# Performance work log

Measured on AMD Instinct MI355X. Metric: run time of the kernel, lower is better.

## Reference

```python
import jax, jax.numpy as jnp
import numpy as np
from jax import lax

DIM = 192
HEADS = 8
HID = int(DIM * 4.0)

def setup_inputs() -> dict:
    key = jax.random.key(0)
    ks = jax.random.split(key, 10)
    b, c, h, w = 4, DIM, 256, DIM  # w must equal dim for the Mlp over last axis
    x = jax.random.normal(ks[0], (b, c, h, w), dtype=jnp.float32)
    return {
        "x": x,
        "ln1_w": jnp.ones((DIM,), jnp.float32),
        "ln1_b": jnp.zeros((DIM,), jnp.float32),
        "temperature": jnp.ones((HEADS, 1, 1), jnp.float32),
        "qkv_w": jax.random.normal(ks[1], (3 * DIM, DIM), jnp.float32) * 0.02,
        "dw_w": jax.random.normal(ks[2], (3 * DIM, 1, 3, 3), jnp.float32) * 0.1,
        "proj_w": jax.random.normal(ks[3], (DIM, DIM), jnp.float32) * 0.02,
        "ln2_w": jnp.ones((DIM,), jnp.float32),
        "ln2_b": jnp.zeros((DIM,), jnp.float32),
        "fc1_w": jax.random.normal(ks[4], (HID, DIM), jnp.float32) * 0.02,
        "fc1_b": jnp.zeros((HID,), jnp.float32),
        "fc2_w": jax.random.normal(ks[5], (DIM, HID), jnp.float32) * 0.02,
        "fc2_b": jnp.zeros((DIM,), jnp.float32),
    }

def _layernorm_chan(x, w, b):
    # WithBias LayerNorm over the channel axis, per spatial location (to_3d -> LN -> to_4d)
    mu = jnp.mean(x, axis=1, keepdims=True)
    var = jnp.mean((x - mu) ** 2, axis=1, keepdims=True)
    y = (x - mu) / jnp.sqrt(var + 1e-5)
    return y * w[None, :, None, None] + b[None, :, None, None]

def _l2norm(x, axis=-1, eps=1e-12):
    n = jnp.sqrt(jnp.sum(x * x, axis=axis, keepdims=True))
    return x / jnp.maximum(n, eps)

def _attention(x, temperature, qkv_w, dw_w, proj_w):
    b, c, h, w = x.shape
    # 1x1 conv (pointwise GEMM) then 3x3 depthwise conv
    qkv = jnp.einsum('oc,bchw->bohw', qkv_w, x)
    qkv = lax.conv_general_dilated(qkv, dw_w, window_strides=(1, 1), padding='SAME',
                                   feature_group_count=3 * c,
                                   dimension_numbers=('NCHW', 'OIHW', 'NCHW'))
    q, k, v = jnp.split(qkv, 3, axis=1)
    ch = c // HEADS
    q = q.reshape(b, HEADS, ch, h * w)
    k = k.reshape(b, HEADS, ch, h * w)
    v = v.reshape(b, HEADS, ch, h * w)
    q = _l2norm(q)
    k = _l2norm(k)
    attn = jnp.einsum('bhcn,bhdn->bhcd', q, k) * temperature  # [b,H,ch,ch] channel attention
    attn = jax.nn.softmax(attn, axis=-1)
    out = jnp.einsum('bhcd,bhdn->bhcn', attn, v).reshape(b, c, h, w)
    return jnp.einsum('oc,bchw->bohw', proj_w, out)

def _mlp(x, fc1_w, fc1_b, fc2_w, fc2_b):
    # nn.Linear applied on the LAST axis (w == dim), matching the original quirk
    h1 = jnp.einsum('bchw,ow->bcho', x, fc1_w) + fc1_b
    h1 = jax.nn.gelu(h1, approximate=False)
    return jnp.einsum('bcho,do->bchd', h1, fc2_w) + fc2_b

def reference(x, ln1_w, ln1_b, temperature, qkv_w, dw_w, proj_w, ln2_w, ln2_b, fc1_w, fc1_b, fc2_w, fc2_b):
    x = x + _attention(_layernorm_chan(x, ln1_w, ln1_b), temperature, qkv_w, dw_w, proj_w)
    x = x + _mlp(_layernorm_chan(x, ln2_w, ln2_b), fc1_w, fc1_b, fc2_w, fc2_b)
    return x
```

## Files before the change

kernel.cpp:

```cpp
#include <hip/hip_runtime.h>
#include <math.h>

#define SSP   49152
#define HDIM  256
#define WDIM  192
#define CDIM  192
#define NHEAD 8
#define CH    24
#define OC3   576
#define HIDF  768
#define NB    4
#define SCCH  24

typedef short bf16x8 __attribute__((ext_vector_type(8)));
typedef short bf16x4 __attribute__((ext_vector_type(4)));
typedef float f32x4  __attribute__((ext_vector_type(4)));

__device__ inline short f2bf(float f) {
  unsigned u = __float_as_uint(f);
  u += 0x7fffu + ((u >> 16) & 1u);
  return (short)(u >> 16);
}
__device__ inline float bf2f(short h) {
  return __uint_as_float(((unsigned)(unsigned short)h) << 16);
}

__device__ inline void gl_lds16(const short* g, short* l) {
  __builtin_amdgcn_global_load_lds(
      (const __attribute__((address_space(1))) unsigned int*)g,
      (__attribute__((address_space(3))) unsigned int*)l, 16, 0, 0);
}

__global__ __launch_bounds__(256) void cvt_bf16(const float* __restrict__ in,
                                                short* __restrict__ out, int n) {
  int i = blockIdx.x * 256 + threadIdx.x;
  if (i < n) out[i] = f2bf(in[i]);
}

template <bool TRANS>
__global__ __launch_bounds__(256) void ln_bf16(const float* __restrict__ x,
                                               const float* __restrict__ w,
                                               const float* __restrict__ bia,
                                               short* __restrict__ outp) {
  __shared__ float xs[192][68];
  __shared__ float ps[4][64], pq[4][64], mus[64], rst[64];
  const int tid = threadIdx.x;
  const int s0 = blockIdx.x * 64;
  const float* xb = x + (size_t)blockIdx.y * CDIM * SSP;
  short* outb = outp + (size_t)blockIdx.y * CDIM * SSP;
#pragma unroll
  for (int it = 0; it < 12; ++it) {
    int u = it * 256 + tid;
    int c = u >> 4, q = u & 15;
    float4 v = *(const float4*)(xb + (size_t)c * SSP + s0 + q * 4);
    *(float4*)&xs[c][q * 4] = v;
  }
  __syncthreads();
  {
    int s = tid & 63, p = tid >> 6;
    float sm = 0.f, sq = 0.f;
    for (int c = p * 48; c < p * 48 + 48; ++c) {
      float v = xs[c][s]; sm += v; sq += v * v;
    }
    ps[p][s] = sm; pq[p][s] = sq;
  }
  __syncthreads();
  if (tid < 64) {
    float sm = ps[0][tid] + ps[1][tid] + ps[2][tid] + ps[3][tid];
    float sq = pq[0][tid] + pq[1][tid] + pq[2][tid] + pq[3][tid];
    float mu = sm * (1.f / CDIM);
    mus[tid] = mu;
    rst[tid] = rsqrtf(sq * (1.f / CDIM) - mu * mu + 1e-5f);
  }
  __syncthreads();
  if (TRANS) {
#pragma unroll
    for (int it = 0; it < 6; ++it) {
      int u = it * 256 + tid;
      int c8 = u >> 6, sr = u & 63;
      float mu = mus[sr], r = rst[sr];
      bf16x8 o;
#pragma unroll
      for (int j = 0; j < 8; ++j) {
        int c = c8 * 8 + j;
        o[j] = f2bf((xs[c][sr] - mu) * r * w[c] + bia[c]);
      }
      *(bf16x8*)(outb + (size_t)(s0 + sr) * CDIM + c8 * 8) = o;
    }
  } else {
#pragma unroll
    for (int it = 0; it < 6; ++it) {
      int u = it * 256 + tid;
      int c = u >> 3, sv = u & 7;
      float wc = w[c], bc = bia[c];
      bf16x8 o;
#pragma unroll
      for (int j = 0; j < 8; ++j) {
        int s = sv * 8 + j;
        o[j] = f2bf((xs[c][s] - mus[s]) * rst[s] * wc + bc);
      }
      *(bf16x8*)(outb + (size_t)c * SSP + s0 + sv * 8) = o;
    }
  }
}

template <bool RESID, bool OUT_BF16>
__global__ __launch_bounds__(256) void mfma_gemm(
    const short* __restrict__ A, const short* __restrict__ B,
    const float* __restrict__ resid, void* __restrict__ Cv,
    int M, int N, int K, long long strideB, long long strideC) {
  __shared__ short As[64 * 32];
  __shared__ short Bs[256 * 32];
  const int tid = threadIdx.x;
  const int m0 = blockIdx.y * 64, n0 = blockIdx.x * 256;
  const long long z = blockIdx.z;
  const short* Bz = B + z * strideB;
  const int w = tid >> 6, lane = tid & 63;
  const int r16 = lane & 15, kg = lane >> 4;
  const int arow = tid >> 2, ac4 = tid & 3;

  f32x4 acc[4][4] = {};

  for (int k0 = 0; k0 < K; k0 += 32) {
    gl_lds16(A + (size_t)(m0 + arow) * K + k0 + ac4 * 8, As + w * 512);
#pragma unroll
    for (int p = 0; p < 4; ++p) {
      int flat = p * 256 + tid;
      int brow = flat >> 2, bc4 = flat & 3;
      gl_lds16(Bz + (size_t)(n0 + brow) * K + k0 + bc4 * 8, Bs + p * 2048 + w * 512);
    }
    __syncthreads();
    bf16x8 af[4], bfr[4];
#pragma unroll
    for (int i = 0; i < 4; ++i)
      af[i] = *(bf16x8*)(&As[(i * 16 + r16) * 32 + kg * 8]);
#pragma unroll
    for (int j = 0; j < 4; ++j)
      bfr[j] = *(bf16x8*)(&Bs[(w * 64 + j * 16 + r16) * 32 + kg * 8]);
#pragma unroll
    for (int i = 0; i < 4; ++i)
#pragma unroll
      for (int j = 0; j < 4; ++j)
        acc[i][j] = __builtin_amdgcn_mfma_f32_16x16x32_bf16(af[i], bfr[j], acc[i][j], 0, 0, 0);
    __syncthreads();
  }

  float* Cf = (float*)Cv + z * strideC;
  short* Ch = (short*)Cv + z * strideC;
  const float* R = RESID ? resid + z * strideC : nullptr;
#pragma unroll
  for (int i = 0; i < 4; ++i) {
#pragma unroll
    for (int j = 0; j < 4; ++j) {
#pragma unroll
      for (int t = 0; t < 4; ++t) {
        int m = m0 + i * 16 + kg * 4 + t;
        int n = n0 + w * 64 + j * 16 + r16;
        float v = acc[i][j][t];
        size_t idx = (size_t)m * N + n;
        if (RESID) v += R[idx];
        if (OUT_BF16) Ch[idx] = f2bf(v); else Cf[idx] = v;
      }
    }
  }
}

__global__ __launch_bounds__(256) void dwconv_tile(const short* __restrict__ in,
                                                   const float* __restrict__ w9,
                                                   short* __restrict__ out) {
  __shared__ short tile[34][208];
  const int tid = threadIdx.x;
  const int ch = blockIdx.x >> 3;
  const int slab = blockIdx.x & 7;
  const int o = ch % OC3;
  const int y0 = slab * 32;
  float wr[9];
#pragma unroll
  for (int i = 0; i < 9; ++i) wr[i] = w9[o * 9 + i];
  const short* ip = in + (size_t)ch * SSP;

  if (tid < 34) { tile[tid][7] = 0; tile[tid][200] = 0; }
#pragma unroll
  for (int i = 0; i < 4; ++i) {
    int idx = i * 256 + tid;
    if (idx < 816) {
      int row = idx / 24, cx = idx - row * 24;
      int gy = y0 + row - 1;
      bf16x8 v = {};
      if (gy >= 0 && gy < HDIM) v = *(const bf16x8*)(ip + gy * WDIM + cx * 8);
      *(bf16x8*)(&tile[row][8 + cx * 8]) = v;
    }
  }
  __syncthreads();

  short* op = out + (size_t)ch * SSP;
#pragma unroll
  for (int g = 0; g < 3; ++g) {
    int G = g * 256 + tid;
    int r = G / 24, cx = G - (G / 24) * 24;
    int cb = cx * 8 + 7;
    float a[10], b[10], c[10];
#pragma unroll
    for (int d = 0; d < 10; ++d) {
      a[d] = bf2f(tile[r][cb + d]);
      b[d] = bf2f(tile[r + 1][cb + d]);
      c[d] = bf2f(tile[r + 2][cb + d]);
    }
    bf16x8 ov;
#pragma unroll
    for (int j = 0; j < 8; ++j) {
      float acc = wr[0] * a[j] + wr[1] * a[j + 1] + wr[2] * a[j + 2]
                + wr[3] * b[j] + wr[4] * b[j + 1] + wr[5] * b[j + 2]
                + wr[6] * c[j] + wr[7] * c[j + 1] + wr[8] * c[j + 2];
      ov[j] = f2bf(acc);
    }
    *(bf16x8*)(op + (y0 + r) * WDIM + cx * 8) = ov;
  }
}

__global__ __launch_bounds__(256) void scores_stage1(const short* __restrict__ D,
                                                     float* __restrict__ pdot,
                                                     float* __restrict__ qss,
                                                     float* __restrict__ kss) {
  int ch = blockIdx.x, h = blockIdx.y, b = blockIdx.z;
  __shared__ float qs[24][260];
  __shared__ float ks[24][260];
  int tid = threadIdx.x;
  int w = tid >> 6, lane = tid & 63;
  int c0 = w * 6;
  float acc[6] = {0.f, 0.f, 0.f, 0.f, 0.f, 0.f};
  float ssacc = 0.f;
  const short* qb = D + ((size_t)b * OC3 + h * CH) * SSP;
  const short* kb = D + ((size_t)b * OC3 + CDIM + h * CH) * SSP;
  for (int it = 0; it < 8; ++it) {
    int s0 = ch * 2048 + it * 256;
#pragma unroll
    for (int p = 0; p < 3; ++p) {
      int u = p * 256 + tid;
      int row = u >> 5, col8 = u & 31;
      bf16x8 qv = *(const bf16x8*)(qb + (size_t)row * SSP + s0 + col8 * 8);
      bf16x8 kv = *(const bf16x8*)(kb + (size_t)row * SSP + s0 + col8 * 8);
#pragma unroll
      for (int j = 0; j < 8; ++j) {
        qs[row][col8 * 8 + j] = bf2f(qv[j]);
        ks[row][col8 * 8 + j] = bf2f(kv[j]);
      }
    }
    __syncthreads();
    if (w < 2 && lane < 24) {
      const float (*src)[260] = (w == 0) ? qs : ks;
      for (int s = 0; s < 256; s += 4) {
        float4 v = *(const float4*)&src[lane][s];
        ssacc += v.x * v.x + v.y * v.y + v.z * v.z + v.w * v.w;
      }
    }
    if (lane < 24) {
      for (int s = 0; s < 256; s += 4) {
        float4 kv = *(float4*)&ks[lane][s];
#pragma unroll
        for (int i = 0; i < 6; ++i) {
          float4 qv = *(float4*)&qs[c0 + i][s];
          acc[i] += qv.x * kv.x + qv.y * kv.y + qv.z * kv.z + qv.w * kv.w;
        }
      }
    }
    __syncthreads();
  }
  if (lane < 24) {
    float* pb = pdot + (size_t)b * (NHEAD * CH * CH * SCCH);
#pragma unroll
    for (int i = 0; i < 6; ++i)
      pb[(((size_t)h * CH + (c0 + i)) * CH + lane) * SCCH + ch] = acc[i];
    if (w == 0) qss[(((size_t)b * NHEAD + h) * CH + lane) * SCCH + ch] = ssacc;
    if (w == 1) kss[(((size_t)b * NHEAD + h) * CH + lane) * SCCH + ch] = ssacc;
  }
}

__global__ void scores_reduce(const float* __restrict__ pdot,
                              const float* __restrict__ qss,
                              const float* __restrict__ kss,
                              const float* __restrict__ temp,
                              float* __restrict__ atn) {
  int c = blockIdx.x, h = blockIdx.y, b = blockIdx.z;
  int tid = threadIdx.x;
  __shared__ float row[24];
  if (tid < 24) {
    const float* p = pdot + (size_t)b * (NHEAD * CH * CH * SCCH) +
                     (((size_t)h * CH + c) * CH + tid) * SCCH;
    float s = 0.f;
#pragma unroll
    for (int i = 0; i < SCCH; ++i) s += p[i];
    const float* pq = qss + (((size_t)b * NHEAD + h) * CH + c) * SCCH;
    const float* pk = kss + (((size_t)b * NHEAD + h) * CH + tid) * SCCH;
    float sq = 0.f, sk = 0.f;
#pragma unroll
    for (int i = 0; i < SCCH; ++i) { sq += pq[i]; sk += pk[i]; }
    float rq = 1.f / fmaxf(sqrtf(sq), 1e-12f);
    float rk = 1.f / fmaxf(sqrtf(sk), 1e-12f);
    row[tid] = s * rq * rk * temp[h];
  }
  __syncthreads();
  if (tid < 24) {
    float mx = -1e30f;
    for (int d = 0; d < 24; ++d) mx = fmaxf(mx, row[d]);
    float sum = 0.f;
    for (int d = 0; d < 24; ++d) sum += expf(row[d] - mx);
    atn[((size_t)b * NHEAD + h) * 576 + c * CH + tid] = expf(row[tid] - mx) / sum;
  }
}

__global__ __launch_bounds__(256) void attn_pv_bf16(const short* __restrict__ D,
                                                    const float* __restrict__ atn,
                                                    short* __restrict__ pvt) {
  int nb = blockIdx.x, h = blockIdx.y, b = blockIdx.z;
  __shared__ float aL[24][24];
  int tid = threadIdx.x;
  const float* ab = atn + ((size_t)b * NHEAD + h) * 576;
  for (int i = tid; i < 576; i += 256) aL[i / 24][i % 24] = ab[i];
  __syncthreads();
  int n = nb * 256 + tid;
  const short* vb = D + ((size_t)b * OC3 + 2 * CDIM + h * CH) * SSP + n;
  float vv[24];
#pragma unroll
  for (int d = 0; d < 24; ++d) vv[d] = bf2f(vb[(size_t)d * SSP]);
  short* ob = pvt + (size_t)b * SSP * CDIM + (size_t)n * CDIM + h * CH;
  bf16x8 o0, o1, o2;
#pragma unroll
  for (int cc = 0; cc < 24; ++cc) {
    float s = 0.f;
#pragma unroll
    for (int d = 0; d < 24; ++d) s += aL[cc][d] * vv[d];
    short bv = f2bf(s);
    if (cc < 8) o0[cc & 7] = bv; else if (cc < 16) o1[cc & 7] = bv; else o2[cc & 7] = bv;
  }
  *(bf16x8*)(ob) = o0;
  *(bf16x8*)(ob + 8) = o1;
  *(bf16x8*)(ob + 16) = o2;
}

__global__ __launch_bounds__(512) void mlp_fused(const short* __restrict__ y2,
                                                 const short* __restrict__ w1,
                                                 const short* __restrict__ w2,
                                                 const float* __restrict__ b1,
                                                 const float* __restrict__ b2,
                                                 float* __restrict__ out) {
  __shared__ short y2s[128 * 200];
  __shared__ short w1s[64 * 200];
  __shared__ short w2s[192 * 72];
  __shared__ short h1s[128 * 72];
  const int tid = threadIdx.x;
  const int m0 = blockIdx.x * 128;
  const int w = tid >> 6, lane = tid & 63;
  const int r16 = lane & 15, kg = lane >> 4;
  const int wm = w >> 1, wn = w & 1;

  const int u0 = tid, u1 = 512 + tid, u2 = 1024 + tid;
  const int s1r[3] = {u0 / 24, u1 / 24, u2 / 24};
  const int s1c[3] = {u0 % 24, u1 % 24, u2 % 24};
  const int s2r[3] = {u0 / 8, u1 / 8, u2 / 8};
  const int s2c[3] = {u0 % 8, u1 % 8, u2 % 8};

#pragma unroll
  for (int it = 0; it < 6; ++it) {
    int u = it * 512 + tid;
    int row = u / 24, cx = u % 24;
    *(bf16x8*)(&y2s[row * 200 + cx * 8]) =
        *(const bf16x8*)(y2 + (size_t)(m0 + row) * CDIM + cx * 8);
  }
#pragma unroll
  for (int it = 0; it < 3; ++it) {
    *(bf16x8*)(&w1s[s1r[it] * 200 + s1c[it] * 8]) =
        *(const bf16x8*)(w1 + (size_t)s1r[it] * CDIM + s1c[it] * 8);
    *(bf16x8*)(&w2s[s2r[it] * 72 + s2c[it] * 8]) =
        *(const bf16x8*)(w2 + (size_t)s2r[it] * HIDF + s2c[it] * 8);
  }
  __syncthreads();

  f32x4 bacc[2][6] = {};
  bf16x8 rw1[3], rw2[3];

  for (int hc = 0; hc < 12; ++hc) {
    if (hc < 11) {
#pragma unroll
      for (int it = 0; it < 3; ++it) {
        rw1[it] = *(const bf16x8*)(w1 + (size_t)((hc + 1) * 64 + s1r[it]) * CDIM + s1c[it] * 8);
        rw2[it] = *(const bf16x8*)(w2 + (size_t)s2r[it] * HIDF + (hc + 1) * 64 + s2c[it] * 8);
      }
    }
    f32x4 pacc[2][2] = {};
#pragma unroll
    for (int ks = 0; ks < 6; ++ks) {
      bf16x8 af[2], bg[2];
#pragma unroll
      for (int i = 0; i < 2; ++i)
        af[i] = *(bf16x8*)(&y2s[(wm * 32 + i * 16 + r16) * 200 + ks * 32 + kg * 8]);
#pragma unroll
      for (int j = 0; j < 2; ++j)
        bg[j] = *(bf16x8*)(&w1s[(wn * 32 + j * 16 + r16) * 200 + ks * 32 + kg * 8]);
#pragma unroll
      for (int i = 0; i < 2; ++i)
#pragma unroll
        for (int j = 0; j < 2; ++j)
          pacc[i][j] = __builtin_amdgcn_mfma_f32_16x16x32_bf16(bg[j], af[i], pacc[i][j], 0, 0, 0);
    }
#pragma unroll
    for (int i = 0; i < 2; ++i) {
      int mr = wm * 32 + i * 16 + r16;
#pragma unroll
      for (int j = 0; j < 2; ++j) {
        int hid0 = wn * 32 + j * 16 + kg * 4;
        bf16x4 pk;
#pragma unroll
        for (int t = 0; t < 4; ++t) {
          float v = pacc[i][j][t] + b1[hc * 64 + hid0 + t];
          v = 0.5f * v * (1.f + erff(v * 0.70710678118654752f));
          pk[t] = f2bf(v);
        }
        *(bf16x4*)(&h1s[mr * 72 + hid0]) = pk;
      }
    }
    __syncthreads();

#pragma unroll
    for (int ks = 0; ks < 2; ++ks) {
      bf16x8 a2[2];
#pragma unroll
      for (int i = 0; i < 2; ++i)
        a2[i] = *(bf16x8*)(&h1s[(wm * 32 + i * 16 + r16) * 72 + ks * 32 + kg * 8]);
#pragma unroll
      for (int j = 0; j < 6; ++j) {
        bf16x8 b2g = *(bf16x8*)(&w2s[(wn * 96 + j * 16 + r16) * 72 + ks * 32 + kg * 8]);
#pragma unroll
        for (int i = 0; i < 2; ++i)
          bacc[i][j] = __builtin_amdgcn_mfma_f32_16x16x32_bf16(a2[i], b2g, bacc[i][j], 0, 0, 0);
      }
    }
    __syncthreads();

    if (hc < 11) {
#pragma unroll
      for (int it = 0; it < 3; ++it) {
        *(bf16x8*)(&w1s[s1r[it] * 200 + s1c[it] * 8]) = rw1[it];
        *(bf16x8*)(&w2s[s2r[it] * 72 + s2c[it] * 8]) = rw2[it];
      }
      __syncthreads();
    }
  }

#pragma unroll
  for (int i = 0; i < 2; ++i)
#pragma unroll
    for (int j = 0; j < 6; ++j)
#pragma unroll
      for (int t = 0; t < 4; ++t) {
        int m = m0 + wm * 32 + i * 16 + kg * 4 + t;
        int n = wn * 96 + j * 16 + r16;
        size_t idx = (size_t)m * CDIM + n;
        out[idx] = bacc[i][j][t] + b2[n] + out[idx];
      }
}

extern "C" void kernel_launch(void* const* d_in, const int* in_sizes, int n_in,
                              void* d_out, int out_size, void* d_ws, size_t ws_size,
                              hipStream_t stream) {
  const float* x      = (const float*)d_in[0];
  const float* ln1_w  = (const float*)d_in[1];
  const float* ln1_b  = (const float*)d_in[2];
  const float* temp   = (const float*)d_in[3];
  const float* qkv_w  = (const float*)d_in[4];
  const float* dw_w   = (const float*)d_in[5];
  const float* proj_w = (const float*)d_in[6];
  const float* ln2_w  = (const float*)d_in[7];
  const float* ln2_b  = (const float*)d_in[8];
  const float* fc1_w  = (const float*)d_in[9];
  const float* fc1_b  = (const float*)d_in[10];
  const float* fc2_w  = (const float*)d_in[11];
  const float* fc2_b  = (const float*)d_in[12];
  float* out = (float*)d_out;

  char* base = (char*)d_ws;
  short* wq  = (short*)base;
  short* wp  = wq + 110592;
  short* w1  = wp + 36864;
  short* w2  = w1 + 147456;
  float* pdot= (float*)(base + 890880);
  float* qss = (float*)(base + 2660352);
  float* kss = (float*)(base + 2734080);
  float* atn = (float*)(base + 2807808);
  short* Dv  = (short*)(base + 4194304);
  short* y1t = Dv;
  short* T   = (short*)(base + 230686720);
  short* pvt = T;
  short* y2  = (short*)(base + 457179136);

  cvt_bf16<<<dim3(432), 256, 0, stream>>>(qkv_w, wq, 110592);
  cvt_bf16<<<dim3(144), 256, 0, stream>>>(proj_w, wp, 36864);
  cvt_bf16<<<dim3(576), 256, 0, stream>>>(fc1_w, w1, 147456);
  cvt_bf16<<<dim3(576), 256, 0, stream>>>(fc2_w, w2, 147456);

  ln_bf16<true><<<dim3(SSP / 64, NB), 256, 0, stream>>>(x, ln1_w, ln1_b, y1t);
  mfma_gemm<false, true><<<dim3(SSP / 256, OC3 / 64, NB), 256, 0, stream>>>(
      wq, y1t, nullptr, T, OC3, SSP, CDIM, (long long)SSP * CDIM, (long long)OC3 * SSP);
  dwconv_tile<<<dim3(NB * OC3 * 8), 256, 0, stream>>>(T, dw_w, Dv);
  scores_stage1<<<dim3(SCCH, NHEAD, NB), 256, 0, stream>>>(Dv, pdot, qss, kss);
  scores_reduce<<<dim3(CH, NHEAD, NB), 64, 0, stream>>>(pdot, qss, kss, temp, atn);
  attn_pv_bf16<<<dim3(SSP / 256, NHEAD, NB), 256, 0, stream>>>(Dv, atn, pvt);
  mfma_gemm<true, false><<<dim3(SSP / 256, CDIM / 64, NB), 256, 0, stream>>>(
      wp, pvt, x, out, CDIM, SSP, CDIM, (long long)SSP * CDIM, (long long)CDIM * SSP);
  ln_bf16<false><<<dim3(SSP / 64, NB), 256, 0, stream>>>(out, ln2_w, ln2_b, y2);
  mlp_fused<<<dim3(196608 / 128), 512, 0, stream>>>(y2, w1, w2, fc1_b, fc2_b, out);
}
```

Baseline: 946.6 us.

## Merge weight casts, double-stage GEMM K loop, keep MLP activations in registers

Replaces the four weight-conversion launches with a single kernel that writes all four bf16 weights into the contiguous workspace. The generic MFMA GEMM now loads two 32-wide K slices per barrier pair, halving the number of synchronisations per tile. The fused MLP kernel drops its LDS copy of the input rows, holds the A fragments in registers, and adds a launch bound to raise occupancy. It also removes the register prefetch of the next weight chunk, so weight loads are no longer overlapped with compute.

```diff
diff --git a/kernel.cpp b/kernel.cpp
--- a/kernel.cpp
+++ b/kernel.cpp
@@ -31,10 +31,18 @@
       (__attribute__((address_space(3))) unsigned int*)l, 16, 0, 0);
 }
 
-__global__ __launch_bounds__(256) void cvt_bf16(const float* __restrict__ in,
-                                                short* __restrict__ out, int n) {
+__global__ __launch_bounds__(256) void cvt_all(const float* __restrict__ s0,
+                                               const float* __restrict__ s1,
+                                               const float* __restrict__ s2,
+                                               const float* __restrict__ s3,
+                                               short* __restrict__ dst) {
   int i = blockIdx.x * 256 + threadIdx.x;
-  if (i < n) out[i] = f2bf(in[i]);
+  float v;
+  if (i < 110592)      v = s0[i];
+  else if (i < 147456) v = s1[i - 110592];
+  else if (i < 294912) v = s2[i - 147456];
+  else                 v = s3[i - 294912];
+  dst[i] = f2bf(v);
 }
 
 template <bool TRANS>
@@ -109,8 +117,8 @@
     const short* __restrict__ A, const short* __restrict__ B,
     const float* __restrict__ resid, void* __restrict__ Cv,
     int M, int N, int K, long long strideB, long long strideC) {
-  __shared__ short As[64 * 32];
-  __shared__ short Bs[256 * 32];
+  __shared__ short As[2][64 * 32];
+  __shared__ short Bs[2][256 * 32];
   const int tid = threadIdx.x;
   const int m0 = blockIdx.y * 64, n0 = blockIdx.x * 256;
   const long long z = blockIdx.z;
@@ -121,27 +129,33 @@
 
   f32x4 acc[4][4] = {};
 
-  for (int k0 = 0; k0 < K; k0 += 32) {
-    gl_lds16(A + (size_t)(m0 + arow) * K + k0 + ac4 * 8, As + w * 512);
-#pragma unroll
-    for (int p = 0; p < 4; ++p) {
-      int flat = p * 256 + tid;
-      int brow = flat >> 2, bc4 = flat & 3;
-      gl_lds16(Bz + (size_t)(n0 + brow) * K + k0 + bc4 * 8, Bs + p * 2048 + w * 512);
-    }
-    __syncthreads();
-    bf16x8 af[4], bfr[4];
-#pragma unroll
-    for (int i = 0; i < 4; ++i)
-      af[i] = *(bf16x8*)(&As[(i * 16 + r16) * 32 + kg * 8]);
-#pragma unroll
-    for (int j = 0; j < 4; ++j)
-      bfr[j] = *(bf16x8*)(&Bs[(w * 64 + j * 16 + r16) * 32 + kg * 8]);
-#pragma unroll
-    for (int i = 0; i < 4; ++i)
+  for (int k0 = 0; k0 < K; k0 += 64) {
+#pragma unroll
+    for (int s = 0; s < 2; ++s) {
+      gl_lds16(A + (size_t)(m0 + arow) * K + k0 + s * 32 + ac4 * 8, As[s] + w * 512);
+#pragma unroll
+      for (int p = 0; p < 4; ++p) {
+        int flat = p * 256 + tid;
+        int brow = flat >> 2, bc4 = flat & 3;
+        gl_lds16(Bz + (size_t)(n0 + brow) * K + k0 + s * 32 + bc4 * 8, Bs[s] + p * 2048 + w * 512);
+      }
+    }
+    __syncthreads();
+#pragma unroll
+    for (int s = 0; s < 2; ++s) {
+      bf16x8 af[4], bfr[4];
+#pragma unroll
+      for (int i = 0; i < 4; ++i)
+        af[i] = *(bf16x8*)(&As[s][(i * 16 + r16) * 32 + kg * 8]);
 #pragma unroll
       for (int j = 0; j < 4; ++j)
-        acc[i][j] = __builtin_amdgcn_mfma_f32_16x16x32_bf16(af[i], bfr[j], acc[i][j], 0, 0, 0);
+        bfr[j] = *(bf16x8*)(&Bs[s][(w * 64 + j * 16 + r16) * 32 + kg * 8]);
+#pragma unroll
+      for (int i = 0; i < 4; ++i)
+#pragma unroll
+        for (int j = 0; j < 4; ++j)
+          acc[i][j] = __builtin_amdgcn_mfma_f32_16x16x32_bf16(af[i], bfr[j], acc[i][j], 0, 0, 0);
+    }
     __syncthreads();
   }
 
@@ -338,13 +352,12 @@
   *(bf16x8*)(ob + 16) = o2;
 }
 
-__global__ __launch_bounds__(512) void mlp_fused(const short* __restrict__ y2,
-                                                 const short* __restrict__ w1,
-                                                 const short* __restrict__ w2,
-                                                 const float* __restrict__ b1,
-                                                 const float* __restrict__ b2,
-                                                 float* __restrict__ out) {
-  __shared__ short y2s[128 * 200];
+__global__ __launch_bounds__(512, 4) void mlp_fused(const short* __restrict__ y2,
+                                                    const short* __restrict__ w1,
+                                                    const short* __restrict__ w2,
+                                                    const float* __restrict__ b1,
+                                                    const float* __restrict__ b2,
+                                                    float* __restrict__ out) {
   __shared__ short w1s[64 * 200];
   __shared__ short w2s[192 * 72];
   __shared__ short h1s[128 * 72];
@@ -360,40 +373,29 @@
   const int s2r[3] = {u0 / 8, u1 / 8, u2 / 8};
   const int s2c[3] = {u0 % 8, u1 % 8, u2 % 8};
 
-#pragma unroll
-  for (int it = 0; it < 6; ++it) {
-    int u = it * 512 + tid;
-    int row = u / 24, cx = u % 24;
-    *(bf16x8*)(&y2s[row * 200 + cx * 8]) =
-        *(const bf16x8*)(y2 + (size_t)(m0 + row) * CDIM + cx * 8);
-  }
-#pragma unroll
-  for (int it = 0; it < 3; ++it) {
-    *(bf16x8*)(&w1s[s1r[it] * 200 + s1c[it] * 8]) =
-        *(const bf16x8*)(w1 + (size_t)s1r[it] * CDIM + s1c[it] * 8);
-    *(bf16x8*)(&w2s[s2r[it] * 72 + s2c[it] * 8]) =
-        *(const bf16x8*)(w2 + (size_t)s2r[it] * HIDF + s2c[it] * 8);
-  }
-  __syncthreads();
+  bf16x8 afr[2][6];
+#pragma unroll
+  for (int ks = 0; ks < 6; ++ks)
+#pragma unroll
+    for (int i = 0; i < 2; ++i)
+      afr[i][ks] = *(const bf16x8*)(y2 + (size_t)(m0 + wm * 32 + i * 16 + r16) * CDIM + ks * 32 + kg * 8);
 
   f32x4 bacc[2][6] = {};
-  bf16x8 rw1[3], rw2[3];
 
   for (int hc = 0; hc < 12; ++hc) {
-    if (hc < 11) {
-#pragma unroll
-      for (int it = 0; it < 3; ++it) {
-        rw1[it] = *(const bf16x8*)(w1 + (size_t)((hc + 1) * 64 + s1r[it]) * CDIM + s1c[it] * 8);
-        rw2[it] = *(const bf16x8*)(w2 + (size_t)s2r[it] * HIDF + (hc + 1) * 64 + s2c[it] * 8);
-      }
-    }
+#pragma unroll
+    for (int it = 0; it < 3; ++it) {
+      *(bf16x8*)(&w1s[s1r[it] * 200 + s1c[it] * 8]) =
+          *(const bf16x8*)(w1 + (size_t)(hc * 64 + s1r[it]) * CDIM + s1c[it] * 8);
+      *(bf16x8*)(&w2s[s2r[it] * 72 + s2c[it] * 8]) =
+          *(const bf16x8*)(w2 + (size_t)s2r[it] * HIDF + hc * 64 + s2c[it] * 8);
+    }
+    __syncthreads();
+
     f32x4 pacc[2][2] = {};
 #pragma unroll
     for (int ks = 0; ks < 6; ++ks) {
-      bf16x8 af[2], bg[2];
-#pragma unroll
-      for (int i = 0; i < 2; ++i)
-        af[i] = *(bf16x8*)(&y2s[(wm * 32 + i * 16 + r16) * 200 + ks * 32 + kg * 8]);
+      bf16x8 bg[2];
 #pragma unroll
       for (int j = 0; j < 2; ++j)
         bg[j] = *(bf16x8*)(&w1s[(wn * 32 + j * 16 + r16) * 200 + ks * 32 + kg * 8]);
@@ -401,7 +403,7 @@
       for (int i = 0; i < 2; ++i)
 #pragma unroll
         for (int j = 0; j < 2; ++j)
-          pacc[i][j] = __builtin_amdgcn_mfma_f32_16x16x32_bf16(bg[j], af[i], pacc[i][j], 0, 0, 0);
+          pacc[i][j] = __builtin_amdgcn_mfma_f32_16x16x32_bf16(bg[j], afr[i][ks], pacc[i][j], 0, 0, 0);
     }
 #pragma unroll
     for (int i = 0; i < 2; ++i) {
@@ -436,15 +438,6 @@
       }
     }
     __syncthreads();
-
-    if (hc < 11) {
-#pragma unroll
-      for (int it = 0; it < 3; ++it) {
-        *(bf16x8*)(&w1s[s1r[it] * 200 + s1c[it] * 8]) = rw1[it];
-        *(bf16x8*)(&w2s[s2r[it] * 72 + s2c[it] * 8]) = rw2[it];
-      }
-      __syncthreads();
-    }
   }
 
 #pragma unroll
@@ -493,10 +486,7 @@
   short* pvt = T;
   short* y2  = (short*)(base + 457179136);
 
-  cvt_bf16<<<dim3(432), 256, 0, stream>>>(qkv_w, wq, 110592);
-  cvt_bf16<<<dim3(144), 256, 0, stream>>>(proj_w, wp, 36864);
-  cvt_bf16<<<dim3(576), 256, 0, stream>>>(fc1_w, w1, 147456);
-  cvt_bf16<<<dim3(576), 256, 0, stream>>>(fc2_w, w2, 147456);
+  cvt_all<<<dim3(1728), 256, 0, stream>>>(qkv_w, proj_w, fc1_w, fc2_w, wq);
 
   ln_bf16<true><<<dim3(SSP / 64, NB), 256, 0, stream>>>(x, ln1_w, ln1_b, y1t);
   mfma_gemm<false, true><<<dim3(SSP / 256, OC3 / 64, NB), 256, 0, stream>>>(
```

Result: slower. 1.019 ms (+7.7%).
